# Kernel optimization log

Hardware: AMD Instinct MI355X
Metric: run time of the kernel (lower is better)

The kernel has to match this reference:

```python
import jax, jax.numpy as jnp
import numpy as np

N, D, E = 16384, 256, 8
H = D // 2  # gate hidden


def setup_inputs() -> dict:
    key = jax.random.key(0)
    ks = jax.random.split(key, 10)
    s = lambda fan_in: 1.0 / np.sqrt(fan_in)
    return {
        "x":   jax.random.normal(ks[0], (N, D), dtype=jnp.float32),
        # gate: Linear(D, D//2) -> ReLU -> Linear(D//2, E) -> Softmax
        "Wg1": jax.random.uniform(ks[1], (D, H), jnp.float32, -s(D), s(D)),
        "bg1": jax.random.uniform(ks[2], (H,), jnp.float32, -s(D), s(D)),
        "Wg2": jax.random.uniform(ks[3], (H, E), jnp.float32, -s(H), s(H)),
        "bg2": jax.random.uniform(ks[4], (E,), jnp.float32, -s(H), s(H)),
        # experts: per-expert Linear(D,D) -> ReLU -> (Dropout eval=identity) -> Linear(D,D)
        "W1": jax.random.uniform(ks[5], (E, D, D), jnp.float32, -s(D), s(D)),
        "b1": jax.random.uniform(ks[6], (E, D), jnp.float32, -s(D), s(D)),
        "W2": jax.random.uniform(ks[7], (E, D, D), jnp.float32, -s(D), s(D)),
        "b2": jax.random.uniform(ks[8], (E, D), jnp.float32, -s(D), s(D)),
    }


def reference(x, Wg1, bg1, Wg2, bg2, W1, b1, W2, b2):
    # gate: [N, E] softmax over experts
    g = jax.nn.softmax(jax.nn.relu(x @ Wg1 + bg1) @ Wg2 + bg2, axis=-1)
    # all experts applied densely via batched GEMMs (fuses the Python loop)
    h = jax.nn.relu(jnp.einsum("nd,edh->neh", x, W1) + b1)  # [N, E, D]
    y = jnp.einsum("neh,ehd->ned", h, W2) + b2              # [N, E, D]
    # weighted combine: sum_e g[n,e] * y[n,e,:]
    return jnp.einsum("ned,ne->nd", y, g)
```

## Files before the change

kernel.cpp:

```cpp
#include <hip/hip_runtime.h>


typedef unsigned short USH;
typedef float f32x4 __attribute__((ext_vector_type(4)));
typedef __bf16 bf16x8 __attribute__((ext_vector_type(8)));

#define AS1 __attribute__((address_space(1)))
#define AS3 __attribute__((address_space(3)))

#define KS 2112

__device__ __forceinline__ USH f2bf(float f) {
  unsigned int u = __float_as_uint(f);
  u += 0x7fffu + ((u >> 16) & 1u);
  return (USH)(u >> 16);
}

__device__ __forceinline__ void gl2lds16(const void* g, void* l) {
  __builtin_amdgcn_global_load_lds((AS1 const void*)g, (AS3 void*)l, 16, 0, 0);
}


__global__ __launch_bounds__(256) void k_prep(
    const float* __restrict__ x,
    const float* __restrict__ Wg1,
    const float* __restrict__ W1,
    const float* __restrict__ W2,  const float* __restrict__ b2,
    USH* __restrict__ xb, USH* __restrict__ wg1t,
    USH* __restrict__ w1t, USH* __restrict__ w2t) {
  __shared__ float T[64][65];
  int b = blockIdx.x, tid = threadIdx.x;

  if (b < 2048) {
    size_t i8 = ((size_t)b * 256 + tid) * 8;
    float4 a = *(const float4*)(x + i8);
    float4 c = *(const float4*)(x + i8 + 4);
    USH v[8];
    v[0] = f2bf(a.x); v[1] = f2bf(a.y); v[2] = f2bf(a.z); v[3] = f2bf(a.w);
    v[4] = f2bf(c.x); v[5] = f2bf(c.y); v[6] = f2bf(c.z); v[7] = f2bf(c.w);
    *(uint4*)(xb + i8) = *(const uint4*)v;
  } else if (b < 2176) {
    int bp = b - 2048;
    int e = bp >> 4, tl = bp & 15;
    int c0 = (tl >> 2) * 64, h0 = (tl & 3) * 64;
    const float* src = W1 + (size_t)e * 65536;
#pragma unroll
    for (int p = 0; p < 4; ++p) {
      int r = p * 16 + (tid >> 4), d4 = (tid & 15) * 4;
      float4 v = *(const float4*)(src + (size_t)(c0 + r) * 256 + h0 + d4);
      T[r][d4] = v.x; T[r][d4 + 1] = v.y; T[r][d4 + 2] = v.z; T[r][d4 + 3] = v.w;
    }
    __syncthreads();
#pragma unroll
    for (int p = 0; p < 4; ++p) {
      int hr = p * 16 + (tid >> 4), c4 = (tid & 15) * 4;
      USH w[4];
#pragma unroll
      for (int j = 0; j < 4; ++j) w[j] = f2bf(T[c4 + j][hr]);
      *(uint2*)(w1t + (size_t)e * 65536 + (size_t)(h0 + hr) * 256 + c0 + c4) = *(const uint2*)w;
    }
  } else if (b < 2184) {
    int bp = b - 2176;
    int c0 = (bp >> 1) * 64, h0 = (bp & 1) * 64;
#pragma unroll
    for (int p = 0; p < 4; ++p) {
      int r = p * 16 + (tid >> 4), d4 = (tid & 15) * 4;
      float4 v = *(const float4*)(Wg1 + (size_t)(c0 + r) * 128 + h0 + d4);
      T[r][d4] = v.x; T[r][d4 + 1] = v.y; T[r][d4 + 2] = v.z; T[r][d4 + 3] = v.w;
    }
    __syncthreads();
#pragma unroll
    for (int p = 0; p < 4; ++p) {
      int hr = p * 16 + (tid >> 4), c4 = (tid & 15) * 4;
      USH w[4];
#pragma unroll
      for (int j = 0; j < 4; ++j) w[j] = f2bf(T[c4 + j][hr]);
      *(uint2*)(wg1t + (size_t)(h0 + hr) * 256 + c0 + c4) = *(const uint2*)w;
    }
  } else if (b < 2312) {
    int bp = b - 2184;
    int e = bp >> 4, tl = bp & 15;
    int h0 = (tl >> 2) * 64, d0 = (tl & 3) * 64;
    const float* src = W2 + (size_t)e * 65536;
#pragma unroll
    for (int p = 0; p < 4; ++p) {
      int r = p * 16 + (tid >> 4), d4 = (tid & 15) * 4;
      float4 v = *(const float4*)(src + (size_t)(h0 + r) * 256 + d0 + d4);
      T[r][d4] = v.x; T[r][d4 + 1] = v.y; T[r][d4 + 2] = v.z; T[r][d4 + 3] = v.w;
    }
    __syncthreads();
#pragma unroll
    for (int p = 0; p < 4; ++p) {
      int dr = p * 16 + (tid >> 4), h4 = (tid & 15) * 4;
      USH w[4];
#pragma unroll
      for (int j = 0; j < 4; ++j) w[j] = f2bf(T[h4 + j][dr]);
      *(uint2*)(w2t + (size_t)(d0 + dr) * KS + e * 256 + h0 + h4) = *(const uint2*)w;
    }
  } else {
    size_t base = (size_t)tid * KS + 2048;
#pragma unroll
    for (int p = 0; p < 16; ++p) {
      USH w[4];
#pragma unroll
      for (int j = 0; j < 4; ++j) {
        int e = p * 4 + j;
        w[j] = (e < 8) ? f2bf(b2[e * 256 + tid]) : (USH)0;
      }
      *(uint2*)(w2t + base + p * 4) = *(const uint2*)w;
    }
  }
}


__global__ __launch_bounds__(256) void k_gate(const USH* __restrict__ xb,
                                              const USH* __restrict__ wg1t,
                                              const float* __restrict__ bg1,
                                              const float* __restrict__ wg2,
                                              const float* __restrict__ bg2,
                                              float* __restrict__ g,
                                              USH* __restrict__ hw) {
  __shared__ __align__(16) USH As[32 * 64];
  __shared__ __align__(16) USH Bs[128 * 64];
  __shared__ float hg[32 * 129];
  __shared__ float bg1s[128];
  __shared__ float w2s[128 * 8];
  __shared__ float b2s[8];
  __shared__ float lg[32 * 8];

  int tid = threadIdx.x;
  int wave = tid >> 6, lane = tid & 63;
  int quad = lane >> 4, l16 = lane & 15;
  int sw = l16 & 7;
  int wr = wave >> 1, wc = wave & 1;
  int rowBase = blockIdx.x * 32;

  for (int t = tid; t < 1024; t += 256) w2s[t] = wg2[t];
  if (tid < 8) b2s[tid] = bg2[tid];
  if (tid < 128) bg1s[tid] = bg1[tid];

  f32x4 acc[4] = {};
  for (int kt = 0; kt < 4; ++kt) {
    int kb = kt * 64;
    {
      int r = tid >> 3, c8 = (tid & 7) ^ (r & 7);
      gl2lds16(xb + (size_t)(rowBase + r) * 256 + kb + c8 * 8, As + (size_t)tid * 8);
    }
#pragma unroll
    for (int c = 0; c < 4; ++c) {
      int i = c * 256 + tid;
      int r = i >> 3, c8 = (i & 7) ^ (r & 7);
      gl2lds16(wg1t + (size_t)r * 256 + kb + c8 * 8, Bs + (size_t)i * 8);
    }
    __syncthreads();
#pragma unroll
    for (int kkc = 0; kkc < 8; kkc += 4) {
      bf16x8 av = *(const bf16x8*)(As + (wr * 16 + l16) * 64 + (((kkc + quad) ^ sw) * 8));
#pragma unroll
      for (int j = 0; j < 4; ++j) {
        bf16x8 bv = *(const bf16x8*)(Bs + (wc * 64 + j * 16 + l16) * 64 + (((kkc + quad) ^ sw) * 8));
        acc[j] = __builtin_amdgcn_mfma_f32_16x16x32_bf16(av, bv, acc[j], 0, 0, 0);
      }
    }
    __syncthreads();
  }

#pragma unroll
  for (int j = 0; j < 4; ++j)
#pragma unroll
    for (int r = 0; r < 4; ++r) {
      int row = wr * 16 + quad * 4 + r;
      int col = wc * 64 + j * 16 + l16;
      hg[row * 129 + col] = fmaxf(acc[j][r] + bg1s[col], 0.0f);
    }
  __syncthreads();

  {
    int row = tid >> 3, p = tid & 7;
    float s = b2s[p];
    for (int k = 0; k < 128; ++k) s += hg[row * 129 + k] * w2s[k * 8 + p];
    lg[row * 8 + p] = s;
  }
  __syncthreads();

  if (tid < 32) {
    float l[8];
    float m = -1e30f;
#pragma unroll
    for (int e = 0; e < 8; ++e) { l[e] = lg[tid * 8 + e]; m = fmaxf(m, l[e]); }
    float s = 0.0f;
#pragma unroll
    for (int e = 0; e < 8; ++e) { l[e] = expf(l[e] - m); s += l[e]; }
    float inv = 1.0f / s;
    size_t grow = rowBase + tid;
#pragma unroll
    for (int e = 0; e < 8; ++e) {
      float ge = l[e] * inv;
      g[grow * 8 + e] = ge;
      hw[grow * KS + 2048 + e] = f2bf(ge);
    }
#pragma unroll
    for (int z = 0; z < 56; ++z) hw[grow * KS + 2056 + z] = 0;
  }
}


__global__ __launch_bounds__(256) void k_stage1(const USH* __restrict__ xb,
                                                const USH* __restrict__ w1t,
                                                const float* __restrict__ b1,
                                                const float* __restrict__ g,
                                                USH* __restrict__ hw) {
  __shared__ __align__(16) USH As[128 * 64];
  __shared__ __align__(16) USH Bs[128 * 64];
  __shared__ float gs[128];
  __shared__ float b1s[128];

  int tid = threadIdx.x;
  int wave = tid >> 6, lane = tid & 63;
  int quad = lane >> 4, l16 = lane & 15;
  int sw = l16 & 7;
  int wr = wave >> 1, wc = wave & 1;
  int rowBase = blockIdx.x * 128;
  int colBase = blockIdx.y * 128;
  int e = blockIdx.z;

  if (tid < 128) {
    gs[tid] = g[(size_t)(rowBase + tid) * 8 + e];
    b1s[tid] = b1[e * 256 + colBase + tid];
  }

  const USH* B = w1t + (size_t)e * 65536;

  f32x4 acc[4][4] = {};
  for (int kt = 0; kt < 4; ++kt) {
    int kb = kt * 64;
#pragma unroll
    for (int c = 0; c < 4; ++c) {
      int i = c * 256 + tid;
      int r = i >> 3, c8 = (i & 7) ^ (r & 7);
      gl2lds16(xb + (size_t)(rowBase + r) * 256 + kb + c8 * 8, As + (size_t)i * 8);
      gl2lds16(B + (size_t)(colBase + r) * 256 + kb + c8 * 8, Bs + (size_t)i * 8);
    }
    __syncthreads();
#pragma unroll
    for (int kkc = 0; kkc < 8; kkc += 4) {
      int cs = ((kkc + quad) ^ sw) * 8;
      bf16x8 av[4], bv[4];
#pragma unroll
      for (int i = 0; i < 4; ++i)
        av[i] = *(const bf16x8*)(As + (wr * 64 + i * 16 + l16) * 64 + cs);
#pragma unroll
      for (int j = 0; j < 4; ++j)
        bv[j] = *(const bf16x8*)(Bs + (wc * 64 + j * 16 + l16) * 64 + cs);
#pragma unroll
      for (int i = 0; i < 4; ++i)
#pragma unroll
        for (int j = 0; j < 4; ++j)
          acc[i][j] = __builtin_amdgcn_mfma_f32_16x16x32_bf16(av[i], bv[j], acc[i][j], 0, 0, 0);
    }
    __syncthreads();
  }

#pragma unroll
  for (int i = 0; i < 4; ++i) {
#pragma unroll
    for (int r = 0; r < 4; ++r) {
      int rl = wr * 64 + i * 16 + quad * 4 + r;
      float gg = gs[rl];
      size_t grow = (size_t)(rowBase + rl);
#pragma unroll
      for (int j = 0; j < 4; ++j) {
        int cl = wc * 64 + j * 16 + l16;
        float v = fmaxf(acc[i][j][r] + b1s[cl], 0.0f) * gg;
        hw[grow * KS + e * 256 + colBase + cl] = f2bf(v);
      }
    }
  }
}


__global__ __launch_bounds__(256) void k_stage2(const USH* __restrict__ hwm,
                                                const USH* __restrict__ w2t,
                                                float* __restrict__ out) {
  __shared__ __align__(16) USH As[64 * 64];
  __shared__ __align__(16) USH Bs[64 * 64];

  int tid = threadIdx.x;
  int wave = tid >> 6, lane = tid & 63;
  int quad = lane >> 4, l16 = lane & 15;
  int sw = l16 & 7;
  int rowBase = blockIdx.x * 64;
  int colBase = blockIdx.y * 64;

  f32x4 acc[4] = {};
  for (int kt = 0; kt < 33; ++kt) {
    int kb = kt * 64;
#pragma unroll
    for (int c = 0; c < 2; ++c) {
      int i = c * 256 + tid;
      int r = i >> 3, c8 = (i & 7) ^ (r & 7);
      gl2lds16(hwm + (size_t)(rowBase + r) * KS + kb + c8 * 8, As + (size_t)i * 8);
      gl2lds16(w2t + (size_t)(colBase + r) * KS + kb + c8 * 8, Bs + (size_t)i * 8);
    }
    __syncthreads();
#pragma unroll
    for (int kkc = 0; kkc < 8; kkc += 4) {
      int cs = ((kkc + quad) ^ sw) * 8;
      bf16x8 av = *(const bf16x8*)(As + (wave * 16 + l16) * 64 + cs);
#pragma unroll
      for (int j = 0; j < 4; ++j) {
        bf16x8 bv = *(const bf16x8*)(Bs + (j * 16 + l16) * 64 + cs);
        acc[j] = __builtin_amdgcn_mfma_f32_16x16x32_bf16(av, bv, acc[j], 0, 0, 0);
      }
    }
    __syncthreads();
  }

#pragma unroll
  for (int j = 0; j < 4; ++j)
#pragma unroll
    for (int r = 0; r < 4; ++r) {
      int row = wave * 16 + quad * 4 + r;
      out[(size_t)(rowBase + row) * 256 + colBase + j * 16 + l16] = acc[j][r];
    }
}


extern "C" void kernel_launch(void* const* d_in, const int* in_sizes, int n_in,
                              void* d_out, int out_size, void* d_ws, size_t ws_size,
                              hipStream_t stream) {
  const float* x   = (const float*)d_in[0];
  const float* Wg1 = (const float*)d_in[1];
  const float* bg1 = (const float*)d_in[2];
  const float* Wg2 = (const float*)d_in[3];
  const float* bg2 = (const float*)d_in[4];
  const float* W1  = (const float*)d_in[5];
  const float* b1  = (const float*)d_in[6];
  const float* W2  = (const float*)d_in[7];
  const float* b2  = (const float*)d_in[8];
  float* out = (float*)d_out;

  char* ws = (char*)d_ws;
  USH*   xb   = (USH*)(ws);
  USH*   w1t  = (USH*)(ws + 8388608);
  USH*   wg1t = (USH*)(ws + 9437184);
  USH*   w2t  = (USH*)(ws + 9502720);
  float* g    = (float*)(ws + 10584064);
  USH*   hw   = (USH*)(ws + 11108352);

  hipLaunchKernelGGL(k_prep, dim3(2313), dim3(256), 0, stream,
                     x, Wg1, W1, W2, b2, xb, wg1t, w1t, w2t);
  hipLaunchKernelGGL(k_gate,   dim3(512),       dim3(256), 0, stream, xb, wg1t, bg1, Wg2, bg2, g, hw);
  hipLaunchKernelGGL(k_stage1, dim3(128, 2, 8), dim3(256), 0, stream, xb, w1t, b1, g, hw);
  hipLaunchKernelGGL(k_stage2, dim3(256, 4),    dim3(256), 0, stream, hw, w2t, out);
}
```

Baseline: 143.4 us.

## Fuse expert stage1 and stage2 GEMMs into one kernel keeping hidden tile in LDS

Replaces the separate stage1 (x@W1 per expert, writing the gated hidden to global memory) and stage2 (hidden@W2 concatenated over experts) kernels with one fused kernel. Each 64-row block keeps its x tile and the per-expert hidden tile in LDS and streams W1/W2 tiles through a double buffer. The b2 bias is now applied through a gate-weighted sum in the epilogue instead of extra K columns. This removes the large hw intermediate round trip and one launch, but the grid shrinks to 256 blocks of 512 threads, each with a long serial loop over experts, which risks underusing the GPU's CUs.

```diff
diff --git a/kernel.cpp b/kernel.cpp
--- a/kernel.cpp
+++ b/kernel.cpp
@@ -7,8 +7,6 @@
 
 #define AS1 __attribute__((address_space(1)))
 #define AS3 __attribute__((address_space(3)))
-
-#define KS 2112
 
 __device__ __forceinline__ USH f2bf(float f) {
   unsigned int u = __float_as_uint(f);
@@ -25,7 +23,7 @@
     const float* __restrict__ x,
     const float* __restrict__ Wg1,
     const float* __restrict__ W1,
-    const float* __restrict__ W2,  const float* __restrict__ b2,
+    const float* __restrict__ W2,
     USH* __restrict__ xb, USH* __restrict__ wg1t,
     USH* __restrict__ w1t, USH* __restrict__ w2t) {
   __shared__ float T[64][65];
@@ -77,7 +75,7 @@
       for (int j = 0; j < 4; ++j) w[j] = f2bf(T[c4 + j][hr]);
       *(uint2*)(wg1t + (size_t)(h0 + hr) * 256 + c0 + c4) = *(const uint2*)w;
     }
-  } else if (b < 2312) {
+  } else {
     int bp = b - 2184;
     int e = bp >> 4, tl = bp & 15;
     int h0 = (tl >> 2) * 64, d0 = (tl & 3) * 64;
@@ -95,19 +93,7 @@
       USH w[4];
 #pragma unroll
       for (int j = 0; j < 4; ++j) w[j] = f2bf(T[h4 + j][dr]);
-      *(uint2*)(w2t + (size_t)(d0 + dr) * KS + e * 256 + h0 + h4) = *(const uint2*)w;
-    }
-  } else {
-    size_t base = (size_t)tid * KS + 2048;
-#pragma unroll
-    for (int p = 0; p < 16; ++p) {
-      USH w[4];
-#pragma unroll
-      for (int j = 0; j < 4; ++j) {
-        int e = p * 4 + j;
-        w[j] = (e < 8) ? f2bf(b2[e * 256 + tid]) : (USH)0;
-      }
-      *(uint2*)(w2t + base + p * 4) = *(const uint2*)w;
+      *(uint2*)(w2t + (size_t)(d0 + dr) * 2048 + e * 256 + h0 + h4) = *(const uint2*)w;
     }
   }
 }
@@ -118,8 +104,7 @@
                                               const float* __restrict__ bg1,
                                               const float* __restrict__ wg2,
                                               const float* __restrict__ bg2,
-                                              float* __restrict__ g,
-                                              USH* __restrict__ hw) {
+                                              float* __restrict__ g) {
   __shared__ __align__(16) USH As[32 * 64];
   __shared__ __align__(16) USH Bs[128 * 64];
   __shared__ float hg[32 * 129];
@@ -194,134 +179,153 @@
     float inv = 1.0f / s;
     size_t grow = rowBase + tid;
 #pragma unroll
-    for (int e = 0; e < 8; ++e) {
-      float ge = l[e] * inv;
-      g[grow * 8 + e] = ge;
-      hw[grow * KS + 2048 + e] = f2bf(ge);
-    }
-#pragma unroll
-    for (int z = 0; z < 56; ++z) hw[grow * KS + 2056 + z] = 0;
-  }
-}
-
-
-__global__ __launch_bounds__(256) void k_stage1(const USH* __restrict__ xb,
-                                                const USH* __restrict__ w1t,
-                                                const float* __restrict__ b1,
-                                                const float* __restrict__ g,
-                                                USH* __restrict__ hw) {
-  __shared__ __align__(16) USH As[128 * 64];
-  __shared__ __align__(16) USH Bs[128 * 64];
-  __shared__ float gs[128];
-  __shared__ float b1s[128];
-
-  int tid = threadIdx.x;
-  int wave = tid >> 6, lane = tid & 63;
-  int quad = lane >> 4, l16 = lane & 15;
-  int sw = l16 & 7;
-  int wr = wave >> 1, wc = wave & 1;
-  int rowBase = blockIdx.x * 128;
-  int colBase = blockIdx.y * 128;
-  int e = blockIdx.z;
-
-  if (tid < 128) {
-    gs[tid] = g[(size_t)(rowBase + tid) * 8 + e];
-    b1s[tid] = b1[e * 256 + colBase + tid];
-  }
-
-  const USH* B = w1t + (size_t)e * 65536;
-
-  f32x4 acc[4][4] = {};
-  for (int kt = 0; kt < 4; ++kt) {
-    int kb = kt * 64;
-#pragma unroll
-    for (int c = 0; c < 4; ++c) {
-      int i = c * 256 + tid;
-      int r = i >> 3, c8 = (i & 7) ^ (r & 7);
-      gl2lds16(xb + (size_t)(rowBase + r) * 256 + kb + c8 * 8, As + (size_t)i * 8);
-      gl2lds16(B + (size_t)(colBase + r) * 256 + kb + c8 * 8, Bs + (size_t)i * 8);
-    }
-    __syncthreads();
-#pragma unroll
-    for (int kkc = 0; kkc < 8; kkc += 4) {
-      int cs = ((kkc + quad) ^ sw) * 8;
-      bf16x8 av[4], bv[4];
-#pragma unroll
-      for (int i = 0; i < 4; ++i)
-        av[i] = *(const bf16x8*)(As + (wr * 64 + i * 16 + l16) * 64 + cs);
-#pragma unroll
-      for (int j = 0; j < 4; ++j)
-        bv[j] = *(const bf16x8*)(Bs + (wc * 64 + j * 16 + l16) * 64 + cs);
-#pragma unroll
-      for (int i = 0; i < 4; ++i)
-#pragma unroll
-        for (int j = 0; j < 4; ++j)
-          acc[i][j] = __builtin_amdgcn_mfma_f32_16x16x32_bf16(av[i], bv[j], acc[i][j], 0, 0, 0);
-    }
-    __syncthreads();
-  }
-
-#pragma unroll
-  for (int i = 0; i < 4; ++i) {
-#pragma unroll
-    for (int r = 0; r < 4; ++r) {
-      int rl = wr * 64 + i * 16 + quad * 4 + r;
-      float gg = gs[rl];
-      size_t grow = (size_t)(rowBase + rl);
-#pragma unroll
-      for (int j = 0; j < 4; ++j) {
-        int cl = wc * 64 + j * 16 + l16;
-        float v = fmaxf(acc[i][j][r] + b1s[cl], 0.0f) * gg;
-        hw[grow * KS + e * 256 + colBase + cl] = f2bf(v);
-      }
-    }
-  }
-}
-
-
-__global__ __launch_bounds__(256) void k_stage2(const USH* __restrict__ hwm,
-                                                const USH* __restrict__ w2t,
-                                                float* __restrict__ out) {
-  __shared__ __align__(16) USH As[64 * 64];
-  __shared__ __align__(16) USH Bs[64 * 64];
+    for (int e = 0; e < 8; ++e) g[grow * 8 + e] = l[e] * inv;
+  }
+}
+
+
+__global__ __launch_bounds__(512) void k_moe(const USH* __restrict__ xb,
+                                             const USH* __restrict__ w1t,
+                                             const USH* __restrict__ w2t,
+                                             const float* __restrict__ b1,
+                                             const float* __restrict__ b2,
+                                             const float* __restrict__ g,
+                                             float* __restrict__ out) {
+  __shared__ __align__(16) USH xs[4 * 64 * 64];
+  __shared__ __align__(16) USH Hs[64 * 256];
+  __shared__ __align__(16) USH Ws[2][256 * 64];
+  __shared__ float b1s[256];
+  __shared__ float b2s[2048];
+  __shared__ float gs[512];
 
   int tid = threadIdx.x;
   int wave = tid >> 6, lane = tid & 63;
   int quad = lane >> 4, l16 = lane & 15;
   int sw = l16 & 7;
   int rowBase = blockIdx.x * 64;
-  int colBase = blockIdx.y * 64;
-
-  f32x4 acc[4] = {};
-  for (int kt = 0; kt < 33; ++kt) {
-    int kb = kt * 64;
-#pragma unroll
-    for (int c = 0; c < 2; ++c) {
-      int i = c * 256 + tid;
-      int r = i >> 3, c8 = (i & 7) ^ (r & 7);
-      gl2lds16(hwm + (size_t)(rowBase + r) * KS + kb + c8 * 8, As + (size_t)i * 8);
-      gl2lds16(w2t + (size_t)(colBase + r) * KS + kb + c8 * 8, Bs + (size_t)i * 8);
-    }
-    __syncthreads();
-#pragma unroll
-    for (int kkc = 0; kkc < 8; kkc += 4) {
-      int cs = ((kkc + quad) ^ sw) * 8;
-      bf16x8 av = *(const bf16x8*)(As + (wave * 16 + l16) * 64 + cs);
+
+#pragma unroll
+  for (int it = 0; it < 4; ++it) {
+    int i = it * 512 + tid;
+    int kt = i >> 9, rem = i & 511;
+    int r = rem >> 3, slot = rem & 7;
+    int c8 = slot ^ (r & 7);
+    gl2lds16(xb + (size_t)(rowBase + r) * 256 + kt * 64 + c8 * 8, xs + (size_t)i * 8);
+  }
+#pragma unroll
+  for (int t = tid; t < 2048; t += 512) b2s[t] = b2[t];
+  gs[tid] = g[(size_t)rowBase * 8 + tid];
+
+  auto STAGE = [&](int T, int bf) {
+    int e = T >> 3;
+    int cb = (T & 3) * 64;
+    const USH* src;
+    size_t stride;
+    if (T & 4) { src = w2t + e * 256 + cb;               stride = 2048; }
+    else       { src = w1t + (size_t)e * 65536 + cb;     stride = 256;  }
+    USH* dst = &Ws[bf][0];
+#pragma unroll
+    for (int it = 0; it < 4; ++it) {
+      int i = it * 512 + tid;
+      int r = i >> 3, slot = i & 7;
+      int c8 = slot ^ (r & 7);
+      gl2lds16(src + (size_t)r * stride + c8 * 8, dst + (size_t)i * 8);
+    }
+  };
+
+  int wh = wave >> 1, wn = wave & 1;
+  int wn2 = wave >> 2, wd = wave & 3;
+
+  f32x4 oacc[2][4] = {};
+  int buf = 0;
+  STAGE(0, 0);
+
+#pragma unroll 1
+  for (int e = 0; e < 8; ++e) {
+    f32x4 hacc[4][2] = {};
+    if (tid < 256) b1s[tid] = b1[e * 256 + tid];
+
+    for (int kt = 0; kt < 4; ++kt) {
+      __syncthreads();
+      int T = e * 8 + kt;
+      if (T < 63) STAGE(T + 1, buf ^ 1);
+      const USH* W = &Ws[buf][0];
+#pragma unroll
+      for (int kkc = 0; kkc < 8; kkc += 4) {
+        int cs = ((kkc + quad) ^ sw) * 8;
+        bf16x8 av[4], bv[2];
+#pragma unroll
+        for (int i = 0; i < 4; ++i)
+          av[i] = *(const bf16x8*)(W + (wh * 64 + i * 16 + l16) * 64 + cs);
+#pragma unroll
+        for (int j = 0; j < 2; ++j)
+          bv[j] = *(const bf16x8*)(xs + kt * 4096 + (wn * 32 + j * 16 + l16) * 64 + cs);
+#pragma unroll
+        for (int i = 0; i < 4; ++i)
+#pragma unroll
+          for (int j = 0; j < 2; ++j)
+            hacc[i][j] = __builtin_amdgcn_mfma_f32_16x16x32_bf16(av[i], bv[j], hacc[i][j], 0, 0, 0);
+      }
+      buf ^= 1;
+    }
+
+#pragma unroll
+    for (int i = 0; i < 4; ++i) {
+      int c8 = i * 2 + (quad >> 1);
+      int hb = wh * 64 + i * 16 + quad * 4;
+#pragma unroll
+      for (int j = 0; j < 2; ++j) {
+        int n = wn * 32 + j * 16 + l16;
+        float gg = gs[n * 8 + e];
+        USH w4[4];
+#pragma unroll
+        for (int r = 0; r < 4; ++r)
+          w4[r] = f2bf(fmaxf(hacc[i][j][r] + b1s[hb + r], 0.0f) * gg);
+        int off = n * 256 + wh * 64 + (c8 ^ (n & 7)) * 8 + (quad & 1) * 4;
+        *(uint2*)(Hs + off) = *(const uint2*)w4;
+      }
+    }
+
+    for (int ht = 0; ht < 4; ++ht) {
+      __syncthreads();
+      int T = e * 8 + 4 + ht;
+      if (T < 63) STAGE(T + 1, buf ^ 1);
+      const USH* W = &Ws[buf][0];
+#pragma unroll
+      for (int kkc = 0; kkc < 8; kkc += 4) {
+        int cs = ((kkc + quad) ^ sw) * 8;
+        bf16x8 av[2], bv[4];
+#pragma unroll
+        for (int i = 0; i < 2; ++i)
+          av[i] = *(const bf16x8*)(Hs + (wn2 * 32 + i * 16 + l16) * 256 + ht * 64 + cs);
+#pragma unroll
+        for (int j = 0; j < 4; ++j)
+          bv[j] = *(const bf16x8*)(W + (wd * 64 + j * 16 + l16) * 64 + cs);
+#pragma unroll
+        for (int i = 0; i < 2; ++i)
+#pragma unroll
+          for (int j = 0; j < 4; ++j)
+            oacc[i][j] = __builtin_amdgcn_mfma_f32_16x16x32_bf16(av[i], bv[j], oacc[i][j], 0, 0, 0);
+      }
+      buf ^= 1;
+    }
+  }
+
+#pragma unroll
+  for (int i = 0; i < 2; ++i)
+#pragma unroll
+    for (int r = 0; r < 4; ++r) {
+      int n = wn2 * 32 + i * 16 + quad * 4 + r;
+      const float* gr = gs + n * 8;
+      size_t grow = (size_t)(rowBase + n) * 256;
 #pragma unroll
       for (int j = 0; j < 4; ++j) {
-        bf16x8 bv = *(const bf16x8*)(Bs + (j * 16 + l16) * 64 + cs);
-        acc[j] = __builtin_amdgcn_mfma_f32_16x16x32_bf16(av, bv, acc[j], 0, 0, 0);
-      }
-    }
-    __syncthreads();
-  }
-
-#pragma unroll
-  for (int j = 0; j < 4; ++j)
-#pragma unroll
-    for (int r = 0; r < 4; ++r) {
-      int row = wave * 16 + quad * 4 + r;
-      out[(size_t)(rowBase + row) * 256 + colBase + j * 16 + l16] = acc[j][r];
+        int d = wd * 64 + j * 16 + l16;
+        float bias = 0.0f;
+#pragma unroll
+        for (int ee = 0; ee < 8; ++ee) bias += gr[ee] * b2s[ee * 256 + d];
+        out[grow + d] = oacc[i][j][r] + bias;
+      }
     }
 }
 
@@ -346,11 +350,11 @@
   USH*   wg1t = (USH*)(ws + 9437184);
   USH*   w2t  = (USH*)(ws + 9502720);
   float* g    = (float*)(ws + 10584064);
-  USH*   hw   = (USH*)(ws + 11108352);
-
-  hipLaunchKernelGGL(k_prep, dim3(2313), dim3(256), 0, stream,
-                     x, Wg1, W1, W2, b2, xb, wg1t, w1t, w2t);
-  hipLaunchKernelGGL(k_gate,   dim3(512),       dim3(256), 0, stream, xb, wg1t, bg1, Wg2, bg2, g, hw);
-  hipLaunchKernelGGL(k_stage1, dim3(128, 2, 8), dim3(256), 0, stream, xb, w1t, b1, g, hw);
-  hipLaunchKernelGGL(k_stage2, dim3(256, 4),    dim3(256), 0, stream, hw, w2t, out);
-}
+
+  hipLaunchKernelGGL(k_prep, dim3(2312), dim3(256), 0, stream,
+                     x, Wg1, W1, W2, xb, wg1t, w1t, w2t);
+  hipLaunchKernelGGL(k_gate, dim3(512), dim3(256), 0, stream,
+                     xb, wg1t, bg1, Wg2, bg2, g);
+  hipLaunchKernelGGL(k_moe, dim3(256), dim3(512), 0, stream,
+                     xb, w1t, w2t, b1, b2, g, out);
+}
```

Result: slower. 149.2 us (+4.0%).
